# Performance work log

Hardware: AMD Instinct MI355X
Metric: run time of the kernel (lower is better)

## Reference

```python
import jax, jax.numpy as jnp
import numpy as np

N_GENERA = 4096
N_RANKS = 6
N_GROUPS = 256  # distinct taxa per rank (fill_max for labels)


def setup_inputs() -> dict:
    key = jax.random.key(0)
    k1, k2 = jax.random.split(key)
    F_genus = jax.random.normal(k1, (1024, N_GENERA), dtype=jnp.float32)
    labels = jax.random.randint(k2, (N_RANKS, N_GENERA), 0, N_GROUPS, dtype=jnp.int32)
    return {"F_genus": F_genus, "labels": labels}


def reference(F_genus, labels):
    # Original computes F_genus @ W_rank where W_rank[i,j] = (label[i]==label[j]).
    # That is exactly: out[b, j] = sum_{i: label[i]==label[j]} F[b, i]
    # i.e. a segment-sum over genus indices followed by a gather back to genera.
    def per_rank(lab):
        # F_genus.T: [N, B]; segment-sum over genera grouped by this rank's label
        seg = jax.ops.segment_sum(F_genus.T, lab, num_segments=N_GROUPS)  # [G, B]
        return seg[lab]  # gather back: [N, B]

    ranks_out = jax.vmap(per_rank)(labels)          # [R, N, B]
    ranks_out = jnp.transpose(ranks_out, (2, 1, 0))  # [B, N, R]
    # concat the identity (genus-level) channel last, matching the original order
    return jnp.concatenate([ranks_out, F_genus[:, :, None]], axis=2)  # [B, N, R+1]
```

## Files before the change

### kernel.cpp

```cpp
#include <hip/hip_runtime.h>

#define N_GENERA 4096
#define N_RANKS 6
#define N_GROUPS 256
#define NCH 7
#define SEG_SZ (N_RANKS * N_GROUPS)
#define EXT_SZ (SEG_SZ + N_GENERA)
#define NF (N_GENERA * NCH)
#define NF4 (NF / 4)

typedef float f32x4 __attribute__((ext_vector_type(4)));

#define WS_IDX_OFF  0
#define WS_OFFS_OFF 98304
#define WS_SIDX_OFF 104704

__global__ __launch_bounds__(256) void prep_kernel(
    const int* __restrict__ labels,
    int* __restrict__ idx,
    int* __restrict__ offs,
    short* __restrict__ sidx)
{
    const int t = threadIdx.x;

    if (blockIdx.x < N_RANKS) {
        const int r = blockIdx.x;
        const int* __restrict__ lab = labels + r * N_GENERA;

        __shared__ int cnt[N_GROUPS];
        __shared__ int scan[N_GROUPS];
        __shared__ int cur[N_GROUPS];

        cnt[t] = 0;
        __syncthreads();
        for (int i = t; i < N_GENERA; i += 256)
            atomicAdd(&cnt[lab[i]], 1);
        __syncthreads();

        int v = cnt[t];
        scan[t] = v;
        __syncthreads();
        #pragma unroll
        for (int s = 1; s < 256; s <<= 1) {
            int add = (t >= s) ? scan[t - s] : 0;
            __syncthreads();
            scan[t] += add;
            __syncthreads();
        }
        int start = scan[t] - v;
        cur[t] = start;
        offs[r * 260 + t] = start;
        if (t == 0) offs[r * 260 + 256] = N_GENERA;
        __syncthreads();
        for (int i = t; i < N_GENERA; i += 256) {
            int p = atomicAdd(&cur[lab[i]], 1);
            idx[r * N_GENERA + p] = i;
        }
    } else {
        const int f = (blockIdx.x - N_RANKS) * 256 + t;
        const int j = f / NCH;
        const int ch = f - j * NCH;
        int v;
        if (ch < N_RANKS)
            v = ch * N_GROUPS + labels[ch * N_GENERA + j];
        else
            v = SEG_SZ + j;
        sidx[f] = (short)v;
    }
}

__global__ __launch_bounds__(512) void fused_kernel(
    const float* __restrict__ F,
    const int* __restrict__ idx,
    const int* __restrict__ offs,
    const short* __restrict__ sidx,
    float* __restrict__ out)
{
    __shared__ float ext[EXT_SZ];
    const int b = blockIdx.x;
    const int t = threadIdx.x;

    const f32x4* Fv = reinterpret_cast<const f32x4*>(F + (size_t)b * N_GENERA);
    f32x4* Flv = reinterpret_cast<f32x4*>(ext + SEG_SZ);
    #pragma unroll
    for (int k = 0; k < 2; ++k) Flv[t + k * 512] = Fv[t + k * 512];
    __syncthreads();

    const float* __restrict__ Fl = ext + SEG_SZ;
    #pragma unroll
    for (int w = 0; w < 3; ++w) {
        const int item = t + w * 512;
        const int r = item >> 8;
        const int g = item & 255;
        const int s1 = offs[r * 260 + g + 1];
        int k = offs[r * 260 + g];
        const int* __restrict__ ip = idx + r * N_GENERA;
        float s = 0.f;
        for (; k + 4 <= s1; k += 4) {
            int i0 = ip[k], i1 = ip[k + 1], i2 = ip[k + 2], i3 = ip[k + 3];
            float a0 = Fl[i0], a1 = Fl[i1], a2 = Fl[i2], a3 = Fl[i3];
            s += (a0 + a1) + (a2 + a3);
        }
        for (; k < s1; ++k) s += Fl[ip[k]];
        ext[item] = s;
    }
    __syncthreads();

    f32x4* __restrict__ op = reinterpret_cast<f32x4*>(out) + (size_t)b * NF4;
    #pragma unroll
    for (int kk = 0; kk < 14; ++kk) {
        const int q = kk * 512 + t;
        short4 s4 = *reinterpret_cast<const short4*>(sidx + q * 4);
        f32x4 v;
        v[0] = ext[s4.x];
        v[1] = ext[s4.y];
        v[2] = ext[s4.z];
        v[3] = ext[s4.w];
        op[q] = v;
    }
}

extern "C" void kernel_launch(void* const* d_in, const int* in_sizes, int n_in,
                              void* d_out, int out_size, void* d_ws, size_t ws_size,
                              hipStream_t stream) {
    const float* F      = (const float*)d_in[0];
    const int*   labels = (const int*)d_in[1];
    float*       out    = (float*)d_out;

    const int B = in_sizes[0] / N_GENERA;
    char* ws = (char*)d_ws;
    int*   idx  = (int*)(ws + WS_IDX_OFF);
    int*   offs = (int*)(ws + WS_OFFS_OFF);
    short* sidx = (short*)(ws + WS_SIDX_OFF);

    const int sidx_blocks = NF / 256;
    prep_kernel<<<dim3(N_RANKS + sidx_blocks), dim3(256), 0, stream>>>(labels, idx, offs, sidx);
    fused_kernel<<<dim3(B), dim3(512), 0, stream>>>(F, idx, offs, sidx, out);
}
```

Baseline: 45.82 us.

## Replace CSR gather-sum with LDS atomic scatter-add segment sums

Drops the counting sort, prefix scan and CSR index lists from the prep kernel. Each genus's six per-rank segment indices are now packed into one uint4. The fused kernel zeroes the segment sums in LDS and scatter-adds each F value into its six segments with shared-memory float atomics, replacing the variable-length per-group gather loops. Loads of F and stores of the output also become nontemporal. This removes load imbalance and the serial prep work, at the cost of LDS atomic contention and a summation order that varies between runs.

```diff
diff --git a/kernel.cpp b/kernel.cpp
--- a/kernel.cpp
+++ b/kernel.cpp
@@ -11,53 +11,32 @@
 
 typedef float f32x4 __attribute__((ext_vector_type(4)));
 
-#define WS_IDX_OFF  0
-#define WS_OFFS_OFF 98304
-#define WS_SIDX_OFF 104704
+#define WS_PK_OFF   0
+#define WS_SIDX_OFF 65536
 
 __global__ __launch_bounds__(256) void prep_kernel(
     const int* __restrict__ labels,
-    int* __restrict__ idx,
-    int* __restrict__ offs,
+    uint* __restrict__ pk,
     short* __restrict__ sidx)
 {
     const int t = threadIdx.x;
 
-    if (blockIdx.x < N_RANKS) {
-        const int r = blockIdx.x;
-        const int* __restrict__ lab = labels + r * N_GENERA;
-
-        __shared__ int cnt[N_GROUPS];
-        __shared__ int scan[N_GROUPS];
-        __shared__ int cur[N_GROUPS];
-
-        cnt[t] = 0;
-        __syncthreads();
-        for (int i = t; i < N_GENERA; i += 256)
-            atomicAdd(&cnt[lab[i]], 1);
-        __syncthreads();
-
-        int v = cnt[t];
-        scan[t] = v;
-        __syncthreads();
-        #pragma unroll
-        for (int s = 1; s < 256; s <<= 1) {
-            int add = (t >= s) ? scan[t - s] : 0;
-            __syncthreads();
-            scan[t] += add;
-            __syncthreads();
-        }
-        int start = scan[t] - v;
-        cur[t] = start;
-        offs[r * 260 + t] = start;
-        if (t == 0) offs[r * 260 + 256] = N_GENERA;
-        __syncthreads();
-        for (int i = t; i < N_GENERA; i += 256) {
-            int p = atomicAdd(&cur[lab[i]], 1);
-            idx[r * N_GENERA + p] = i;
-        }
+    if (blockIdx.x < 16) {
+        const int i = blockIdx.x * 256 + t;
+        const int l0 = labels[0 * N_GENERA + i];
+        const int l1 = labels[1 * N_GENERA + i];
+        const int l2 = labels[2 * N_GENERA + i];
+        const int l3 = labels[3 * N_GENERA + i];
+        const int l4 = labels[4 * N_GENERA + i];
+        const int l5 = labels[5 * N_GENERA + i];
+        uint4 w;
+        w.x = (uint)(l0)        | ((uint)(256  + l1) << 16);
+        w.y = (uint)(512 + l2)  | ((uint)(768  + l3) << 16);
+        w.z = (uint)(1024 + l4) | ((uint)(1280 + l5) << 16);
+        w.w = 0u;
+        reinterpret_cast<uint4*>(pk)[i] = w;
     } else {
-        const int f = (blockIdx.x - N_RANKS) * 256 + t;
+        const int f = (blockIdx.x - 16) * 256 + t;
         const int j = f / NCH;
         const int ch = f - j * NCH;
         int v;
@@ -71,8 +50,7 @@
 
 __global__ __launch_bounds__(512) void fused_kernel(
     const float* __restrict__ F,
-    const int* __restrict__ idx,
-    const int* __restrict__ offs,
+    const uint* __restrict__ pk,
     const short* __restrict__ sidx,
     float* __restrict__ out)
 {
@@ -80,29 +58,41 @@
     const int b = blockIdx.x;
     const int t = threadIdx.x;
 
+    ext[t]        = 0.f;
+    ext[t + 512]  = 0.f;
+    ext[t + 1024] = 0.f;
+
     const f32x4* Fv = reinterpret_cast<const f32x4*>(F + (size_t)b * N_GENERA);
+    const f32x4 f0 = __builtin_nontemporal_load(Fv + t);
+    const f32x4 f1 = __builtin_nontemporal_load(Fv + t + 512);
     f32x4* Flv = reinterpret_cast<f32x4*>(ext + SEG_SZ);
-    #pragma unroll
-    for (int k = 0; k < 2; ++k) Flv[t + k * 512] = Fv[t + k * 512];
+    Flv[t]       = f0;
+    Flv[t + 512] = f1;
+
     __syncthreads();
 
-    const float* __restrict__ Fl = ext + SEG_SZ;
+    const uint4* pk4 = reinterpret_cast<const uint4*>(pk);
     #pragma unroll
-    for (int w = 0; w < 3; ++w) {
-        const int item = t + w * 512;
-        const int r = item >> 8;
-        const int g = item & 255;
-        const int s1 = offs[r * 260 + g + 1];
-        int k = offs[r * 260 + g];
-        const int* __restrict__ ip = idx + r * N_GENERA;
-        float s = 0.f;
-        for (; k + 4 <= s1; k += 4) {
-            int i0 = ip[k], i1 = ip[k + 1], i2 = ip[k + 2], i3 = ip[k + 3];
-            float a0 = Fl[i0], a1 = Fl[i1], a2 = Fl[i2], a3 = Fl[i3];
-            s += (a0 + a1) + (a2 + a3);
-        }
-        for (; k < s1; ++k) s += Fl[ip[k]];
-        ext[item] = s;
+    for (int u = 0; u < 4; ++u) {
+        const uint4 p = pk4[4 * t + u];
+        const float fv = f0[u];
+        atomicAdd(&ext[p.x & 0xffffu], fv);
+        atomicAdd(&ext[p.x >> 16],     fv);
+        atomicAdd(&ext[p.y & 0xffffu], fv);
+        atomicAdd(&ext[p.y >> 16],     fv);
+        atomicAdd(&ext[p.z & 0xffffu], fv);
+        atomicAdd(&ext[p.z >> 16],     fv);
+    }
+    #pragma unroll
+    for (int u = 0; u < 4; ++u) {
+        const uint4 p = pk4[2048 + 4 * t + u];
+        const float fv = f1[u];
+        atomicAdd(&ext[p.x & 0xffffu], fv);
+        atomicAdd(&ext[p.x >> 16],     fv);
+        atomicAdd(&ext[p.y & 0xffffu], fv);
+        atomicAdd(&ext[p.y >> 16],     fv);
+        atomicAdd(&ext[p.z & 0xffffu], fv);
+        atomicAdd(&ext[p.z >> 16],     fv);
     }
     __syncthreads();
 
@@ -116,7 +106,7 @@
         v[1] = ext[s4.y];
         v[2] = ext[s4.z];
         v[3] = ext[s4.w];
-        op[q] = v;
+        __builtin_nontemporal_store(v, op + q);
     }
 }
 
@@ -129,11 +119,10 @@
 
     const int B = in_sizes[0] / N_GENERA;
     char* ws = (char*)d_ws;
-    int*   idx  = (int*)(ws + WS_IDX_OFF);
-    int*   offs = (int*)(ws + WS_OFFS_OFF);
+    uint*  pk   = (uint*)(ws + WS_PK_OFF);
     short* sidx = (short*)(ws + WS_SIDX_OFF);
 
     const int sidx_blocks = NF / 256;
-    prep_kernel<<<dim3(N_RANKS + sidx_blocks), dim3(256), 0, stream>>>(labels, idx, offs, sidx);
-    fused_kernel<<<dim3(B), dim3(512), 0, stream>>>(F, idx, offs, sidx, out);
+    prep_kernel<<<dim3(16 + sidx_blocks), dim3(256), 0, stream>>>(labels, pk, sidx);
+    fused_kernel<<<dim3(B), dim3(512), 0, stream>>>(F, pk, sidx, out);
 }
```

New measurement: 146.9 us. 221% more time.

## Process two batch rows per block with interleaved float2 LDS layout

Applied to the files above, without the earlier changes.

Each block now handles two batch rows, storing them interleaved as float2 in shared memory so the index loads (idx, offs, sidx) and LDS gathers are amortized across both rows. Global loads and stores also switch to nontemporal builtins to avoid cache pollution for streaming data. This halves the grid to 512 blocks and doubles LDS per block (about 44KB), which may reduce occupancy. It also adds a zero-init of the segment region.

```diff
diff --git a/kernel.cpp b/kernel.cpp
--- a/kernel.cpp
+++ b/kernel.cpp
@@ -76,47 +76,68 @@
     const short* __restrict__ sidx,
     float* __restrict__ out)
 {
-    __shared__ float ext[EXT_SZ];
-    const int b = blockIdx.x;
+    __shared__ float2 ext2[EXT_SZ];
+    const int b0 = blockIdx.x * 2;
     const int t = threadIdx.x;
 
-    const f32x4* Fv = reinterpret_cast<const f32x4*>(F + (size_t)b * N_GENERA);
-    f32x4* Flv = reinterpret_cast<f32x4*>(ext + SEG_SZ);
+    const float2 z2 = {0.f, 0.f};
+    ext2[t] = z2; ext2[t + 512] = z2; ext2[t + 1024] = z2;
+
+    const f32x4* Fv0 = reinterpret_cast<const f32x4*>(F + (size_t)b0 * N_GENERA);
+    const f32x4* Fv1 = reinterpret_cast<const f32x4*>(F + (size_t)(b0 + 1) * N_GENERA);
+    f32x4* Flv = reinterpret_cast<f32x4*>(ext2 + SEG_SZ);
     #pragma unroll
-    for (int k = 0; k < 2; ++k) Flv[t + k * 512] = Fv[t + k * 512];
+    for (int k = 0; k < 2; ++k) {
+        const f32x4 a = __builtin_nontemporal_load(Fv0 + t + k * 512);
+        const f32x4 c = __builtin_nontemporal_load(Fv1 + t + k * 512);
+        f32x4 lo, hi;
+        lo[0] = a[0]; lo[1] = c[0]; lo[2] = a[1]; lo[3] = c[1];
+        hi[0] = a[2]; hi[1] = c[2]; hi[2] = a[3]; hi[3] = c[3];
+        Flv[2 * (t + k * 512)]     = lo;
+        Flv[2 * (t + k * 512) + 1] = hi;
+    }
     __syncthreads();
 
-    const float* __restrict__ Fl = ext + SEG_SZ;
+    const float2* __restrict__ Fl2 = ext2 + SEG_SZ;
     #pragma unroll
     for (int w = 0; w < 3; ++w) {
         const int item = t + w * 512;
         const int r = item >> 8;
         const int g = item & 255;
-        const int s1 = offs[r * 260 + g + 1];
+        const int e = offs[r * 260 + g + 1];
         int k = offs[r * 260 + g];
         const int* __restrict__ ip = idx + r * N_GENERA;
-        float s = 0.f;
-        for (; k + 4 <= s1; k += 4) {
+        float sa = 0.f, sb = 0.f;
+        for (; k + 4 <= e; k += 4) {
             int i0 = ip[k], i1 = ip[k + 1], i2 = ip[k + 2], i3 = ip[k + 3];
-            float a0 = Fl[i0], a1 = Fl[i1], a2 = Fl[i2], a3 = Fl[i3];
-            s += (a0 + a1) + (a2 + a3);
+            float2 v0 = Fl2[i0], v1 = Fl2[i1], v2 = Fl2[i2], v3 = Fl2[i3];
+            sa += (v0.x + v1.x) + (v2.x + v3.x);
+            sb += (v0.y + v1.y) + (v2.y + v3.y);
         }
-        for (; k < s1; ++k) s += Fl[ip[k]];
-        ext[item] = s;
+        for (; k < e; ++k) {
+            float2 v = Fl2[ip[k]];
+            sa += v.x; sb += v.y;
+        }
+        float2 sp; sp.x = sa; sp.y = sb;
+        ext2[item] = sp;
     }
     __syncthreads();
 
-    f32x4* __restrict__ op = reinterpret_cast<f32x4*>(out) + (size_t)b * NF4;
+    f32x4* __restrict__ op0 = reinterpret_cast<f32x4*>(out) + (size_t)b0 * NF4;
+    f32x4* __restrict__ op1 = op0 + NF4;
     #pragma unroll
     for (int kk = 0; kk < 14; ++kk) {
         const int q = kk * 512 + t;
         short4 s4 = *reinterpret_cast<const short4*>(sidx + q * 4);
-        f32x4 v;
-        v[0] = ext[s4.x];
-        v[1] = ext[s4.y];
-        v[2] = ext[s4.z];
-        v[3] = ext[s4.w];
-        op[q] = v;
+        float2 p0 = ext2[s4.x];
+        float2 p1 = ext2[s4.y];
+        float2 p2 = ext2[s4.z];
+        float2 p3 = ext2[s4.w];
+        f32x4 va, vb;
+        va[0] = p0.x; va[1] = p1.x; va[2] = p2.x; va[3] = p3.x;
+        vb[0] = p0.y; vb[1] = p1.y; vb[2] = p2.y; vb[3] = p3.y;
+        __builtin_nontemporal_store(va, op0 + q);
+        __builtin_nontemporal_store(vb, op1 + q);
     }
 }
 
@@ -135,5 +156,5 @@
 
     const int sidx_blocks = NF / 256;
     prep_kernel<<<dim3(N_RANKS + sidx_blocks), dim3(256), 0, stream>>>(labels, idx, offs, sidx);
-    fused_kernel<<<dim3(B), dim3(512), 0, stream>>>(F, idx, offs, sidx, out);
+    fused_kernel<<<dim3(B / 2), dim3(512), 0, stream>>>(F, idx, offs, sidx, out);
 }
```

After: 43.05 us. 6.0% less time.
